# Kernel optimization log

Measured on AMD Instinct MI355X. Metric: run time of the kernel, lower is better.

The kernel has to match this reference:

```python
import jax, jax.numpy as jnp
import numpy as np

N_NODES = 100000


def setup_inputs() -> dict:
    key = jax.random.key(0)
    k1, k2, k3 = jax.random.split(key, 3)
    Cin, Cout, E = 128, 128, 1600000
    x = jax.random.normal(k1, (N_NODES, Cin), dtype=jnp.float32)
    edge_index = jax.random.randint(k2, (2, E), 0, N_NODES, dtype=jnp.int64)
    W = jax.random.normal(k3, (Cin, Cout), dtype=jnp.float32) * 0.05
    b = jnp.zeros((Cout,), dtype=jnp.float32)
    return {"x": x, "edge_index": edge_index, "W": W, "b": b}


def reference(x, edge_index, W, b):
    # GCNConv with self-loops + symmetric normalization, then SiLU.
    N = x.shape[0]
    loops = jnp.arange(N, dtype=edge_index.dtype)
    src = jnp.concatenate([edge_index[0], loops])  # [E+N]
    dst = jnp.concatenate([edge_index[1], loops])  # [E+N]

    h = x @ W  # [N, Cout]

    # degree on dst column (includes self-loops)
    deg = jax.ops.segment_sum(jnp.ones_like(dst, dtype=h.dtype), dst, num_segments=N)
    dis = jnp.where(deg > 0, jax.lax.rsqrt(jnp.maximum(deg, 1.0)), 0.0)  # deg^-1/2, inf->0
    norm = dis[src] * dis[dst]  # [E+N]

    msgs = h[src] * norm[:, None]  # gather + scale
    out = jax.ops.segment_sum(msgs, dst, num_segments=N) + b  # scatter-add
    return jax.nn.silu(out)
```

## Files before the change

### kernel.cpp

```cpp
#include <hip/hip_runtime.h>
#include <math.h>

#define C      128
#define C2U    64
#define BSH    7
#define BNODES 128
#define CHUNKE 6144
#define PADMAX (BNODES * 3)

typedef __attribute__((ext_vector_type(8))) short bf16x8;
typedef __attribute__((ext_vector_type(4))) float f32x4;

union UV { uint4 u; bf16x8 h; };

__device__ __forceinline__ unsigned int f2bf(float f) {
    unsigned int u = __float_as_uint(f);
    return (u + 0x7fffu + ((u >> 16) & 1u)) >> 16;
}
__device__ __forceinline__ float bflo(unsigned int v) { return __uint_as_float(v << 16); }
__device__ __forceinline__ float bfhi(unsigned int v) { return __uint_as_float(v & 0xffff0000u); }

__global__ __launch_bounds__(256) void ngl_chist_kernel(
        const int* __restrict__ dst, int E, int NBUCK, int NBLK, int* __restrict__ cnt) {
    extern __shared__ int h[];
    for (int i = threadIdx.x; i < NBUCK; i += 256) h[i] = 0;
    __syncthreads();
    int base = blockIdx.x * CHUNKE;
    int end = base + CHUNKE; if (end > E) end = E;
    for (int i = base + threadIdx.x; i < end; i += 256)
        atomicAdd(&h[dst[i] >> BSH], 1);
    __syncthreads();
    for (int i = threadIdx.x; i < NBUCK; i += 256)
        cnt[i * NBLK + blockIdx.x] = h[i];
}

__global__ __launch_bounds__(256) void ngl_s1_kernel(const int* __restrict__ in,
                                                     int* __restrict__ bsum, int M,
                                                     const float* __restrict__ W,
                                                     unsigned int* __restrict__ Wt) {
    int g = blockIdx.x * 256 + threadIdx.x;
    if (g < C * C2U) {
        int col = g >> 6, k2 = g & 63;
        float w0 = W[(2 * k2) * C + col];
        float w1 = W[(2 * k2 + 1) * C + col];
        Wt[col * C2U + k2] = f2bf(w0) | (f2bf(w1) << 16);
    }

    __shared__ int red[256];
    int t = threadIdx.x;
    int base = blockIdx.x * 1024 + t * 4;
    int s = 0;
    #pragma unroll
    for (int j = 0; j < 4; ++j) {
        int i = base + j;
        if (i < M) s += in[i];
    }
    red[t] = s;
    __syncthreads();
    for (int o = 128; o > 0; o >>= 1) {
        if (t < o) red[t] += red[t + o];
        __syncthreads();
    }
    if (t == 0) bsum[blockIdx.x] = red[0];
}

__global__ __launch_bounds__(256) void ngl_s2_kernel(
        const int* __restrict__ in, const int* __restrict__ bsum,
        int* __restrict__ out, int M, int NB) {
    __shared__ int pre[256];
    __shared__ int red[256];
    int t = threadIdx.x;
    pre[t] = (t < NB) ? bsum[t] : 0;
    __syncthreads();
    for (int o = 1; o < 256; o <<= 1) {
        int v = 0;
        if (t >= o) v = pre[t - o];
        __syncthreads();
        if (t >= o) pre[t] += v;
        __syncthreads();
    }
    int boff = (blockIdx.x == 0) ? 0 : pre[blockIdx.x - 1];

    int base = blockIdx.x * 1024 + t * 4;
    int v[4];
    int s = 0;
    #pragma unroll
    for (int j = 0; j < 4; ++j) {
        int i = base + j;
        v[j] = (i < M) ? in[i] : 0;
        s += v[j];
    }
    red[t] = s;
    __syncthreads();
    for (int o = 1; o < 256; o <<= 1) {
        int u = 0;
        if (t >= o) u = red[t - o];
        __syncthreads();
        if (t >= o) red[t] += u;
        __syncthreads();
    }
    int run = boff + ((t == 0) ? 0 : red[t - 1]);
    #pragma unroll
    for (int j = 0; j < 4; ++j) {
        int i = base + j;
        if (i < M) {
            out[i] = run;
            run += v[j];
        }
    }
}

__global__ __launch_bounds__(256) void ngl_cscat_kernel(
        const int* __restrict__ src, const int* __restrict__ dst, int E,
        int NBUCK, int NBLK, const int* __restrict__ cntoff,
        unsigned int* __restrict__ pk) {
    extern __shared__ int cur[];
    int blk = blockIdx.x;
    for (int i = threadIdx.x; i < NBUCK; i += 256) cur[i] = cntoff[i * NBLK + blk];
    __syncthreads();
    int base = blk * CHUNKE;
    int end = base + CHUNKE; if (end > E) end = E;
    for (int i = base + threadIdx.x; i < end; i += 256) {
        int d = dst[i];
        int b = d >> BSH;
        int pos = atomicAdd(&cur[b], 1);
        pk[pos] = (unsigned int)src[i] | ((unsigned int)(d & (BNODES - 1)) << 17);
    }
}

__global__ __launch_bounds__(256) void ngl_fcomb_kernel(
        const unsigned int* __restrict__ pk, const int* __restrict__ cntoff,
        int NBLK, int E, int N,
        int* __restrict__ deg, float* __restrict__ dis,
        int* __restrict__ offset, int* __restrict__ payload) {
    __shared__ int h[BNODES];
    __shared__ int sc[BNODES];
    __shared__ int cur[BNODES];
    int b = blockIdx.x, nb = gridDim.x;
    int s = cntoff[b * NBLK];
    int e = (b + 1 < nb) ? cntoff[(b + 1) * NBLK] : E;
    int pbase = s + b * PADMAX;
    int t = threadIdx.x;
    if (t < BNODES) h[t] = 0;
    __syncthreads();
    for (int i = s + t; i < e; i += 256)
        atomicAdd(&h[pk[i] >> 17], 1);
    __syncthreads();
    if (t < BNODES) sc[t] = (h[t] + 3) & ~3;
    __syncthreads();
    for (int o = 1; o < BNODES; o <<= 1) {
        int v = 0;
        if (t < BNODES && t >= o) v = sc[t - o];
        __syncthreads();
        if (t < BNODES && t >= o) sc[t] += v;
        __syncthreads();
    }
    if (t < BNODES) {
        int pc = (h[t] + 3) & ~3;
        int ex = sc[t] - pc;
        cur[t] = ex;
        int n = b * BNODES + t;
        if (n < N) {
            int dv = h[t];
            deg[n] = dv;
            dis[n] = rsqrtf((float)(dv + 1));
            offset[n] = pbase + ex;
        }
    }
    __syncthreads();
    for (int i = s + t; i < e; i += 256) {
        unsigned int p = pk[i];
        int loc = (int)(p >> 17);
        int pos = pbase + atomicAdd(&cur[loc], 1);
        payload[pos] = (int)(p & 0x1FFFFu);
    }
    __syncthreads();
    if (t < BNODES) {
        for (int j = cur[t]; j < sc[t]; ++j)
            payload[pbase + j] = N;
    }
}

__global__ __launch_bounds__(256) void ngl_cvtx_kernel(
        const float4* __restrict__ x4, const float* __restrict__ dis,
        uint4* __restrict__ xh4, int N, int nt) {
    int t = blockIdx.x * blockDim.x + threadIdx.x;
    if (t >= nt) return;
    int node = t >> 4;
    int q = t & 15;
    if (node >= N) {
        xh4[node * 16 + q] = make_uint4(0, 0, 0, 0);
        return;
    }
    float d = dis[node];
    float4 a = x4[node * 32 + q * 2], b = x4[node * 32 + q * 2 + 1];
    uint4 o;
    o.x = f2bf(a.x * d) | (f2bf(a.y * d) << 16);
    o.y = f2bf(a.z * d) | (f2bf(a.w * d) << 16);
    o.z = f2bf(b.x * d) | (f2bf(b.y * d) << 16);
    o.w = f2bf(b.z * d) | (f2bf(b.w * d) << 16);
    xh4[node * 16 + q] = o;
}

__global__ __launch_bounds__(256) void ngl_gather_kernel(
        const unsigned int* __restrict__ xh, const float* __restrict__ dis,
        const int* __restrict__ offset, const int* __restrict__ deg,
        const int* __restrict__ payload, unsigned int* __restrict__ agg, int N) {
    int node = blockIdx.x * 4 + (threadIdx.x >> 6);
    int lane = threadIdx.x & 63;
    if (node >= N) return;

    unsigned int sv = xh[(unsigned int)(node * C2U + lane)];
    float accx = bflo(sv);
    float accy = bfhi(sv);

    int beg = offset[node];
    int cntp = (deg[node] + 3) & ~3;

    if (cntp > 0) {
        int e0 = payload[beg + 0], e1 = payload[beg + 1];
        int e2 = payload[beg + 2], e3 = payload[beg + 3];
        int i = 0;
        while (true) {
            int c0 = e0, c1 = e1, c2 = e2, c3 = e3;
            int nb = beg + i + 4;
            if (i + 8 <= cntp) {
                e0 = payload[nb + 0]; e1 = payload[nb + 1];
                e2 = payload[nb + 2]; e3 = payload[nb + 3];
            }
            unsigned int v0 = xh[(unsigned int)(c0 * C2U + lane)];
            unsigned int v1 = xh[(unsigned int)(c1 * C2U + lane)];
            unsigned int v2 = xh[(unsigned int)(c2 * C2U + lane)];
            unsigned int v3 = xh[(unsigned int)(c3 * C2U + lane)];
            accx += bflo(v0); accy += bfhi(v0);
            accx += bflo(v1); accy += bfhi(v1);
            accx += bflo(v2); accy += bfhi(v2);
            accx += bflo(v3); accy += bfhi(v3);
            i += 4;
            if (i >= cntp) break;
        }
    }
    float dn = dis[node];
    agg[(unsigned int)(node * C2U + lane)] = f2bf(accx * dn) | (f2bf(accy * dn) << 16);
}

__device__ __forceinline__ float silu1(float v) {
    return v / (1.0f + __expf(-v));
}

__global__ __launch_bounds__(256, 2) void ngl_mfma_gemm_kernel(
        const uint4* __restrict__ agg4, const uint4* __restrict__ wt4,
        const float* __restrict__ bias, float* __restrict__ out,
        int N, int tiles_total) {
    int wid  = threadIdx.x >> 6;
    int lane = threadIdx.x & 63;
    int r  = lane & 15;
    int kg = lane >> 4;

    bf16x8 bfr[8][4];
    #pragma unroll
    for (int nt = 0; nt < 8; ++nt) {
        #pragma unroll
        for (int kk = 0; kk < 4; ++kk) {
            UV u; u.u = wt4[(nt * 16 + r) * 16 + kk * 4 + kg];
            bfr[nt][kk] = u.h;
        }
    }
    float bv[8];
    #pragma unroll
    for (int nt = 0; nt < 8; ++nt) bv[nt] = bias[nt * 16 + r];

    for (int tile = blockIdx.x * 4 + wid; tile < tiles_total; tile += gridDim.x * 4) {
        int row0 = tile * 16;
        int arow = row0 + r;

        bf16x8 afr[4];
        #pragma unroll
        for (int kk = 0; kk < 4; ++kk) {
            UV u;
            u.u = (arow < N) ? agg4[(long long)arow * 16 + kk * 4 + kg]
                             : make_uint4(0, 0, 0, 0);
            afr[kk] = u.h;
        }

        f32x4 acc[8];
        #pragma unroll
        for (int nt = 0; nt < 8; ++nt) acc[nt] = (f32x4){0.f, 0.f, 0.f, 0.f};

        #pragma unroll
        for (int kk = 0; kk < 4; ++kk) {
            #pragma unroll
            for (int nt = 0; nt < 8; ++nt) {
                acc[nt] = __builtin_amdgcn_mfma_f32_16x16x32_bf16(
                    afr[kk], bfr[nt][kk], acc[nt], 0, 0, 0);
            }
        }

        #pragma unroll
        for (int nt = 0; nt < 8; ++nt) {
            #pragma unroll
            for (int j = 0; j < 4; ++j) {
                int rr = row0 + kg * 4 + j;
                if (rr < N)
                    __builtin_nontemporal_store(
                        silu1(acc[nt][j] + bv[nt]),
                        &out[(long long)rr * C + nt * 16 + r]);
            }
        }
    }
}

extern "C" void kernel_launch(void* const* d_in, const int* in_sizes, int n_in,
                              void* d_out, int out_size, void* d_ws, size_t ws_size,
                              hipStream_t stream) {
    const float* x = (const float*)d_in[0];
    const int*   ei = (const int*)d_in[1];
    const float* W = (const float*)d_in[2];
    const float* b = (const float*)d_in[3];

    int N = in_sizes[0] / C;
    int E = in_sizes[1] / 2;
    const int* src = ei;
    const int* dst = ei + E;

    int NBUCK = (N + BNODES - 1) / BNODES;
    int NBLK  = (E + CHUNKE - 1) / CHUNKE;
    int M     = NBUCK * NBLK;
    int NB2   = (M + 1023) / 1024;

    char* ws = (char*)d_ws;
    size_t off = 0;
    unsigned int* xh = (unsigned int*)(ws + off);  off += (size_t)(N + 1) * C * 2;
    unsigned int* agg = (unsigned int*)(ws + off); off += (size_t)N * C * 2;
    unsigned int* pk = (unsigned int*)(ws + off);  off += (size_t)E * 4;
    int* payload = (int*)(ws + off);               off += ((size_t)E + (size_t)NBUCK * PADMAX + 1024) * 4;
    int* cnt = (int*)(ws + off);                   off += (size_t)M * 4;
    int* cntoff = (int*)(ws + off);                off += (size_t)M * 4;
    int* s1sum = (int*)(ws + off);                 off += 1024 * 4;
    int* deg = (int*)(ws + off);                   off += (size_t)N * 4;
    int* offset = (int*)(ws + off);                off += (size_t)N * 4;
    float* dis = (float*)(ws + off);               off += (size_t)N * 4;
    unsigned int* Wt = (unsigned int*)(ws + off);  off += (size_t)C * C2U * 4;

    ngl_chist_kernel<<<NBLK, 256, NBUCK * 4, stream>>>(dst, E, NBUCK, NBLK, cnt);
    ngl_s1_kernel<<<NB2, 256, 0, stream>>>(cnt, s1sum, M, W, Wt);
    ngl_s2_kernel<<<NB2, 256, 0, stream>>>(cnt, s1sum, cntoff, M, NB2);
    ngl_cscat_kernel<<<NBLK, 256, NBUCK * 4, stream>>>(src, dst, E, NBUCK, NBLK, cntoff, pk);
    ngl_fcomb_kernel<<<NBUCK, 256, 0, stream>>>(pk, cntoff, NBLK, E, N,
                                                deg, dis, offset, payload);

    int ntx = (N + 1) * 16;
    ngl_cvtx_kernel<<<(ntx + 255) / 256, 256, 0, stream>>>(
        (const float4*)x, dis, (uint4*)xh, N, ntx);

    ngl_gather_kernel<<<(N + 3) / 4, 256, 0, stream>>>(
        xh, dis, offset, deg, payload, agg, N);

    int tiles = (N + 15) / 16;
    ngl_mfma_gemm_kernel<<<512, 256, 0, stream>>>(
        (const uint4*)agg, (const uint4*)Wt, b, (float*)d_out, N, tiles);
}
```

Baseline: 155.0 us.

## Fuse x conversion into CSR build and fuse gather with MFMA GEMM

Folds the x-to-bf16 scaling pass into the per-bucket CSR combine kernel, using degree scales held in shared memory. It also merges the neighbor gather with the MFMA projection: each block aggregates 16 rows into a swizzled LDS tile, then four waves each compute two output column tiles. This removes two launches and the bf16 agg round trip through global memory. The cost is that every block reloads its W fragments, and the GEMM can no longer run as a persistent grid that keeps weights in registers.

```diff
diff --git a/kernel.cpp b/kernel.cpp
--- a/kernel.cpp
+++ b/kernel.cpp
@@ -37,7 +37,8 @@
 __global__ __launch_bounds__(256) void ngl_s1_kernel(const int* __restrict__ in,
                                                      int* __restrict__ bsum, int M,
                                                      const float* __restrict__ W,
-                                                     unsigned int* __restrict__ Wt) {
+                                                     unsigned int* __restrict__ Wt,
+                                                     uint4* __restrict__ xh4, int N) {
     int g = blockIdx.x * 256 + threadIdx.x;
     if (g < C * C2U) {
         int col = g >> 6, k2 = g & 63;
@@ -45,6 +46,8 @@
         float w1 = W[(2 * k2 + 1) * C + col];
         Wt[col * C2U + k2] = f2bf(w0) | (f2bf(w1) << 16);
     }
+    if (blockIdx.x == 0 && threadIdx.x < 16)
+        xh4[(long long)N * 16 + threadIdx.x] = make_uint4(0, 0, 0, 0);
 
     __shared__ int red[256];
     int t = threadIdx.x;
@@ -132,10 +135,12 @@
         const unsigned int* __restrict__ pk, const int* __restrict__ cntoff,
         int NBLK, int E, int N,
         int* __restrict__ deg, float* __restrict__ dis,
-        int* __restrict__ offset, int* __restrict__ payload) {
+        int* __restrict__ offset, int* __restrict__ payload,
+        const float4* __restrict__ x4, uint4* __restrict__ xh4) {
     __shared__ int h[BNODES];
     __shared__ int sc[BNODES];
     __shared__ int cur[BNODES];
+    __shared__ float dl[BNODES];
     int b = blockIdx.x, nb = gridDim.x;
     int s = cntoff[b * NBLK];
     int e = (b + 1 < nb) ? cntoff[(b + 1) * NBLK] : E;
@@ -160,10 +165,12 @@
         int ex = sc[t] - pc;
         cur[t] = ex;
         int n = b * BNODES + t;
+        int dv = h[t];
+        float d = rsqrtf((float)(dv + 1));
+        dl[t] = d;
         if (n < N) {
-            int dv = h[t];
             deg[n] = dv;
-            dis[n] = rsqrtf((float)(dv + 1));
+            dis[n] = d;
             offset[n] = pbase + ex;
         }
     }
@@ -179,133 +186,122 @@
         for (int j = cur[t]; j < sc[t]; ++j)
             payload[pbase + j] = N;
     }
-}
-
-__global__ __launch_bounds__(256) void ngl_cvtx_kernel(
-        const float4* __restrict__ x4, const float* __restrict__ dis,
-        uint4* __restrict__ xh4, int N, int nt) {
-    int t = blockIdx.x * blockDim.x + threadIdx.x;
-    if (t >= nt) return;
-    int node = t >> 4;
     int q = t & 15;
-    if (node >= N) {
-        xh4[node * 16 + q] = make_uint4(0, 0, 0, 0);
-        return;
-    }
-    float d = dis[node];
-    float4 a = x4[node * 32 + q * 2], b = x4[node * 32 + q * 2 + 1];
-    uint4 o;
-    o.x = f2bf(a.x * d) | (f2bf(a.y * d) << 16);
-    o.y = f2bf(a.z * d) | (f2bf(a.w * d) << 16);
-    o.z = f2bf(b.x * d) | (f2bf(b.y * d) << 16);
-    o.w = f2bf(b.z * d) | (f2bf(b.w * d) << 16);
-    xh4[node * 16 + q] = o;
-}
-
-__global__ __launch_bounds__(256) void ngl_gather_kernel(
+    #pragma unroll
+    for (int it = 0; it < 8; ++it) {
+        int rloc = it * 16 + (t >> 4);
+        int n = b * BNODES + rloc;
+        if (n < N) {
+            float d = dl[rloc];
+            float4 a = x4[(long long)n * 32 + q * 2];
+            float4 bb = x4[(long long)n * 32 + q * 2 + 1];
+            uint4 o;
+            o.x = f2bf(a.x * d) | (f2bf(a.y * d) << 16);
+            o.y = f2bf(a.z * d) | (f2bf(a.w * d) << 16);
+            o.z = f2bf(bb.x * d) | (f2bf(bb.y * d) << 16);
+            o.w = f2bf(bb.z * d) | (f2bf(bb.w * d) << 16);
+            xh4[(long long)n * 16 + q] = o;
+        }
+    }
+}
+
+__device__ __forceinline__ float silu1(float v) {
+    return v / (1.0f + __expf(-v));
+}
+
+__global__ __launch_bounds__(256) void ngl_gg_kernel(
         const unsigned int* __restrict__ xh, const float* __restrict__ dis,
         const int* __restrict__ offset, const int* __restrict__ deg,
-        const int* __restrict__ payload, unsigned int* __restrict__ agg, int N) {
-    int node = blockIdx.x * 4 + (threadIdx.x >> 6);
-    int lane = threadIdx.x & 63;
-    if (node >= N) return;
-
-    unsigned int sv = xh[(unsigned int)(node * C2U + lane)];
-    float accx = bflo(sv);
-    float accy = bfhi(sv);
-
-    int beg = offset[node];
-    int cntp = (deg[node] + 3) & ~3;
-
-    if (cntp > 0) {
-        int e0 = payload[beg + 0], e1 = payload[beg + 1];
-        int e2 = payload[beg + 2], e3 = payload[beg + 3];
-        int i = 0;
-        while (true) {
-            int c0 = e0, c1 = e1, c2 = e2, c3 = e3;
-            int nb = beg + i + 4;
-            if (i + 8 <= cntp) {
-                e0 = payload[nb + 0]; e1 = payload[nb + 1];
-                e2 = payload[nb + 2]; e3 = payload[nb + 3];
-            }
-            unsigned int v0 = xh[(unsigned int)(c0 * C2U + lane)];
-            unsigned int v1 = xh[(unsigned int)(c1 * C2U + lane)];
-            unsigned int v2 = xh[(unsigned int)(c2 * C2U + lane)];
-            unsigned int v3 = xh[(unsigned int)(c3 * C2U + lane)];
-            accx += bflo(v0); accy += bfhi(v0);
-            accx += bflo(v1); accy += bfhi(v1);
-            accx += bflo(v2); accy += bfhi(v2);
-            accx += bflo(v3); accy += bfhi(v3);
-            i += 4;
-            if (i >= cntp) break;
-        }
-    }
-    float dn = dis[node];
-    agg[(unsigned int)(node * C2U + lane)] = f2bf(accx * dn) | (f2bf(accy * dn) << 16);
-}
-
-__device__ __forceinline__ float silu1(float v) {
-    return v / (1.0f + __expf(-v));
-}
-
-__global__ __launch_bounds__(256, 2) void ngl_mfma_gemm_kernel(
-        const uint4* __restrict__ agg4, const uint4* __restrict__ wt4,
-        const float* __restrict__ bias, float* __restrict__ out,
-        int N, int tiles_total) {
+        const int* __restrict__ payload,
+        const uint4* __restrict__ wt4, const float* __restrict__ bias,
+        float* __restrict__ out, int N) {
+    __shared__ unsigned int xs[16 * 64];
     int wid  = threadIdx.x >> 6;
     int lane = threadIdx.x & 63;
     int r  = lane & 15;
     int kg = lane >> 4;
 
-    bf16x8 bfr[8][4];
-    #pragma unroll
-    for (int nt = 0; nt < 8; ++nt) {
+    bf16x8 bfr[2][4];
+    float bv[2];
+    #pragma unroll
+    for (int n2 = 0; n2 < 2; ++n2) {
+        int nt = wid * 2 + n2;
         #pragma unroll
         for (int kk = 0; kk < 4; ++kk) {
             UV u; u.u = wt4[(nt * 16 + r) * 16 + kk * 4 + kg];
-            bfr[nt][kk] = u.h;
-        }
-    }
-    float bv[8];
-    #pragma unroll
-    for (int nt = 0; nt < 8; ++nt) bv[nt] = bias[nt * 16 + r];
-
-    for (int tile = blockIdx.x * 4 + wid; tile < tiles_total; tile += gridDim.x * 4) {
-        int row0 = tile * 16;
-        int arow = row0 + r;
-
-        bf16x8 afr[4];
+            bfr[n2][kk] = u.h;
+        }
+        bv[n2] = bias[nt * 16 + r];
+    }
+
+    int row0 = blockIdx.x * 16;
+
+    #pragma unroll
+    for (int j = 0; j < 4; ++j) {
+        int row = wid * 4 + j;
+        int node = row0 + row;
+        float accx = 0.f, accy = 0.f;
+        if (node < N) {
+            unsigned int sv = xh[(unsigned int)(node * C2U + lane)];
+            accx = bflo(sv);
+            accy = bfhi(sv);
+            int beg = offset[node];
+            int cntp = (deg[node] + 3) & ~3;
+            if (cntp > 0) {
+                int e0 = payload[beg + 0], e1 = payload[beg + 1];
+                int e2 = payload[beg + 2], e3 = payload[beg + 3];
+                int i = 0;
+                while (true) {
+                    int c0 = e0, c1 = e1, c2 = e2, c3 = e3;
+                    int nb = beg + i + 4;
+                    if (i + 8 <= cntp) {
+                        e0 = payload[nb + 0]; e1 = payload[nb + 1];
+                        e2 = payload[nb + 2]; e3 = payload[nb + 3];
+                    }
+                    unsigned int v0 = xh[(unsigned int)(c0 * C2U + lane)];
+                    unsigned int v1 = xh[(unsigned int)(c1 * C2U + lane)];
+                    unsigned int v2 = xh[(unsigned int)(c2 * C2U + lane)];
+                    unsigned int v3 = xh[(unsigned int)(c3 * C2U + lane)];
+                    accx += bflo(v0); accy += bfhi(v0);
+                    accx += bflo(v1); accy += bfhi(v1);
+                    accx += bflo(v2); accy += bfhi(v2);
+                    accx += bflo(v3); accy += bfhi(v3);
+                    i += 4;
+                    if (i >= cntp) break;
+                }
+            }
+            float dn = dis[node];
+            accx *= dn; accy *= dn;
+        }
+        xs[row * 64 + ((lane + row * 4) & 63)] = f2bf(accx) | (f2bf(accy) << 16);
+    }
+    __syncthreads();
+
+    bf16x8 afr[4];
+    #pragma unroll
+    for (int kk = 0; kk < 4; ++kk) {
+        UV u;
+        u.u = *(const uint4*)&xs[r * 64 + ((kk * 16 + kg * 4 + r * 4) & 63)];
+        afr[kk] = u.h;
+    }
+    f32x4 acc[2];
+    acc[0] = (f32x4){0.f, 0.f, 0.f, 0.f};
+    acc[1] = (f32x4){0.f, 0.f, 0.f, 0.f};
+    #pragma unroll
+    for (int kk = 0; kk < 4; ++kk) {
+        acc[0] = __builtin_amdgcn_mfma_f32_16x16x32_bf16(afr[kk], bfr[0][kk], acc[0], 0, 0, 0);
+        acc[1] = __builtin_amdgcn_mfma_f32_16x16x32_bf16(afr[kk], bfr[1][kk], acc[1], 0, 0, 0);
+    }
+    #pragma unroll
+    for (int n2 = 0; n2 < 2; ++n2) {
+        int colbase = (wid * 2 + n2) * 16 + r;
         #pragma unroll
-        for (int kk = 0; kk < 4; ++kk) {
-            UV u;
-            u.u = (arow < N) ? agg4[(long long)arow * 16 + kk * 4 + kg]
-                             : make_uint4(0, 0, 0, 0);
-            afr[kk] = u.h;
-        }
-
-        f32x4 acc[8];
-        #pragma unroll
-        for (int nt = 0; nt < 8; ++nt) acc[nt] = (f32x4){0.f, 0.f, 0.f, 0.f};
-
-        #pragma unroll
-        for (int kk = 0; kk < 4; ++kk) {
-            #pragma unroll
-            for (int nt = 0; nt < 8; ++nt) {
-                acc[nt] = __builtin_amdgcn_mfma_f32_16x16x32_bf16(
-                    afr[kk], bfr[nt][kk], acc[nt], 0, 0, 0);
-            }
-        }
-
-        #pragma unroll
-        for (int nt = 0; nt < 8; ++nt) {
-            #pragma unroll
-            for (int j = 0; j < 4; ++j) {
-                int rr = row0 + kg * 4 + j;
-                if (rr < N)
-                    __builtin_nontemporal_store(
-                        silu1(acc[nt][j] + bv[nt]),
-                        &out[(long long)rr * C + nt * 16 + r]);
-            }
+        for (int j = 0; j < 4; ++j) {
+            int rr = row0 + kg * 4 + j;
+            if (rr < N)
+                __builtin_nontemporal_store(
+                    silu1(acc[n2][j] + bv[n2]),
+                    &out[(unsigned int)(rr * C + colbase)]);
         }
     }
 }
@@ -331,7 +327,6 @@
     char* ws = (char*)d_ws;
     size_t off = 0;
     unsigned int* xh = (unsigned int*)(ws + off);  off += (size_t)(N + 1) * C * 2;
-    unsigned int* agg = (unsigned int*)(ws + off); off += (size_t)N * C * 2;
     unsigned int* pk = (unsigned int*)(ws + off);  off += (size_t)E * 4;
     int* payload = (int*)(ws + off);               off += ((size_t)E + (size_t)NBUCK * PADMAX + 1024) * 4;
     int* cnt = (int*)(ws + off);                   off += (size_t)M * 4;
@@ -343,20 +338,14 @@
     unsigned int* Wt = (unsigned int*)(ws + off);  off += (size_t)C * C2U * 4;
 
     ngl_chist_kernel<<<NBLK, 256, NBUCK * 4, stream>>>(dst, E, NBUCK, NBLK, cnt);
-    ngl_s1_kernel<<<NB2, 256, 0, stream>>>(cnt, s1sum, M, W, Wt);
+    ngl_s1_kernel<<<NB2, 256, 0, stream>>>(cnt, s1sum, M, W, Wt, (uint4*)xh, N);
     ngl_s2_kernel<<<NB2, 256, 0, stream>>>(cnt, s1sum, cntoff, M, NB2);
     ngl_cscat_kernel<<<NBLK, 256, NBUCK * 4, stream>>>(src, dst, E, NBUCK, NBLK, cntoff, pk);
     ngl_fcomb_kernel<<<NBUCK, 256, 0, stream>>>(pk, cntoff, NBLK, E, N,
-                                                deg, dis, offset, payload);
-
-    int ntx = (N + 1) * 16;
-    ngl_cvtx_kernel<<<(ntx + 255) / 256, 256, 0, stream>>>(
-        (const float4*)x, dis, (uint4*)xh, N, ntx);
-
-    ngl_gather_kernel<<<(N + 3) / 4, 256, 0, stream>>>(
-        xh, dis, offset, deg, payload, agg, N);
+                                                deg, dis, offset, payload,
+                                                (const float4*)x, (uint4*)xh);
 
     int tiles = (N + 15) / 16;
-    ngl_mfma_gemm_kernel<<<512, 256, 0, stream>>>(
-        (const uint4*)agg, (const uint4*)Wt, b, (float*)d_out, N, tiles);
-}
+    ngl_gg_kernel<<<tiles, 256, 0, stream>>>(
+        xh, dis, offset, deg, payload, (const uint4*)Wt, b, (float*)d_out, N);
+}
```

After: 155.7 us. No clear change (+0.5%).

## Reorder GEMM before aggregation, fusing x conversion into GEMM and SiLU into gather

Applied to the files above, without the earlier changes.

Switches from aggregate-then-transform to transform-then-aggregate. The bf16 conversion of x (scaled by deg^-1/2) now happens inside the MFMA GEMM, which writes h in bf16. The gather kernel then aggregates h rows and applies the destination norm, bias and SiLU, writing the final output directly. This drops the separate cvtx kernel and the agg intermediate round-trip, one launch overall. In exchange, h is rounded to bf16 after the matmul instead of before it, which changes numerics slightly; the 2-byte scattered stores in the GEMM epilogue may be inefficient.

```diff
diff --git a/kernel.cpp b/kernel.cpp
--- a/kernel.cpp
+++ b/kernel.cpp
@@ -37,7 +37,8 @@
 __global__ __launch_bounds__(256) void ngl_s1_kernel(const int* __restrict__ in,
                                                      int* __restrict__ bsum, int M,
                                                      const float* __restrict__ W,
-                                                     unsigned int* __restrict__ Wt) {
+                                                     unsigned int* __restrict__ Wt,
+                                                     uint4* __restrict__ hh4, int N) {
     int g = blockIdx.x * 256 + threadIdx.x;
     if (g < C * C2U) {
         int col = g >> 6, k2 = g & 63;
@@ -45,6 +46,8 @@
         float w1 = W[(2 * k2 + 1) * C + col];
         Wt[col * C2U + k2] = f2bf(w0) | (f2bf(w1) << 16);
     }
+    if (blockIdx.x == 0 && threadIdx.x < 16)
+        hh4[(long long)N * 16 + threadIdx.x] = make_uint4(0, 0, 0, 0);
 
     __shared__ int red[256];
     int t = threadIdx.x;
@@ -181,36 +184,86 @@
     }
 }
 
-__global__ __launch_bounds__(256) void ngl_cvtx_kernel(
+__global__ __launch_bounds__(256, 2) void ngl_gemmcvt_kernel(
         const float4* __restrict__ x4, const float* __restrict__ dis,
-        uint4* __restrict__ xh4, int N, int nt) {
-    int t = blockIdx.x * blockDim.x + threadIdx.x;
-    if (t >= nt) return;
-    int node = t >> 4;
-    int q = t & 15;
-    if (node >= N) {
-        xh4[node * 16 + q] = make_uint4(0, 0, 0, 0);
-        return;
-    }
-    float d = dis[node];
-    float4 a = x4[node * 32 + q * 2], b = x4[node * 32 + q * 2 + 1];
-    uint4 o;
-    o.x = f2bf(a.x * d) | (f2bf(a.y * d) << 16);
-    o.y = f2bf(a.z * d) | (f2bf(a.w * d) << 16);
-    o.z = f2bf(b.x * d) | (f2bf(b.y * d) << 16);
-    o.w = f2bf(b.z * d) | (f2bf(b.w * d) << 16);
-    xh4[node * 16 + q] = o;
+        const uint4* __restrict__ wt4,
+        unsigned short* __restrict__ hh, int N, int tiles_total) {
+    int wid  = threadIdx.x >> 6;
+    int lane = threadIdx.x & 63;
+    int r  = lane & 15;
+    int kg = lane >> 4;
+
+    bf16x8 bfr[8][4];
+    #pragma unroll
+    for (int nt = 0; nt < 8; ++nt) {
+        #pragma unroll
+        for (int kk = 0; kk < 4; ++kk) {
+            UV u; u.u = wt4[(nt * 16 + r) * 16 + kk * 4 + kg];
+            bfr[nt][kk] = u.h;
+        }
+    }
+
+    for (int tile = blockIdx.x * 4 + wid; tile < tiles_total; tile += gridDim.x * 4) {
+        int row0 = tile * 16;
+        int arow = row0 + r;
+        float d = (arow < N) ? dis[arow] : 0.f;
+
+        bf16x8 afr[4];
+        #pragma unroll
+        for (int kk = 0; kk < 4; ++kk) {
+            float4 a = make_float4(0, 0, 0, 0), bb = make_float4(0, 0, 0, 0);
+            if (arow < N) {
+                a  = x4[(long long)arow * 32 + kk * 8 + kg * 2];
+                bb = x4[(long long)arow * 32 + kk * 8 + kg * 2 + 1];
+            }
+            UV u;
+            u.u.x = f2bf(a.x * d) | (f2bf(a.y * d) << 16);
+            u.u.y = f2bf(a.z * d) | (f2bf(a.w * d) << 16);
+            u.u.z = f2bf(bb.x * d) | (f2bf(bb.y * d) << 16);
+            u.u.w = f2bf(bb.z * d) | (f2bf(bb.w * d) << 16);
+            afr[kk] = u.h;
+        }
+
+        f32x4 acc[8];
+        #pragma unroll
+        for (int nt = 0; nt < 8; ++nt) acc[nt] = (f32x4){0.f, 0.f, 0.f, 0.f};
+
+        #pragma unroll
+        for (int kk = 0; kk < 4; ++kk) {
+            #pragma unroll
+            for (int nt = 0; nt < 8; ++nt) {
+                acc[nt] = __builtin_amdgcn_mfma_f32_16x16x32_bf16(
+                    afr[kk], bfr[nt][kk], acc[nt], 0, 0, 0);
+            }
+        }
+
+        #pragma unroll
+        for (int nt = 0; nt < 8; ++nt) {
+            #pragma unroll
+            for (int j = 0; j < 4; ++j) {
+                int rr = row0 + kg * 4 + j;
+                if (rr < N)
+                    hh[(long long)rr * C + nt * 16 + r] =
+                        (unsigned short)f2bf(acc[nt][j]);
+            }
+        }
+    }
+}
+
+__device__ __forceinline__ float silu1(float v) {
+    return v / (1.0f + __expf(-v));
 }
 
 __global__ __launch_bounds__(256) void ngl_gather_kernel(
-        const unsigned int* __restrict__ xh, const float* __restrict__ dis,
+        const unsigned int* __restrict__ hh, const float* __restrict__ dis,
         const int* __restrict__ offset, const int* __restrict__ deg,
-        const int* __restrict__ payload, unsigned int* __restrict__ agg, int N) {
+        const int* __restrict__ payload, const float* __restrict__ bias,
+        float* __restrict__ out, int N) {
     int node = blockIdx.x * 4 + (threadIdx.x >> 6);
     int lane = threadIdx.x & 63;
     if (node >= N) return;
 
-    unsigned int sv = xh[(unsigned int)(node * C2U + lane)];
+    unsigned int sv = hh[(unsigned int)(node * C2U + lane)];
     float accx = bflo(sv);
     float accy = bfhi(sv);
 
@@ -228,10 +281,10 @@
                 e0 = payload[nb + 0]; e1 = payload[nb + 1];
                 e2 = payload[nb + 2]; e3 = payload[nb + 3];
             }
-            unsigned int v0 = xh[(unsigned int)(c0 * C2U + lane)];
-            unsigned int v1 = xh[(unsigned int)(c1 * C2U + lane)];
-            unsigned int v2 = xh[(unsigned int)(c2 * C2U + lane)];
-            unsigned int v3 = xh[(unsigned int)(c3 * C2U + lane)];
+            unsigned int v0 = hh[(unsigned int)(c0 * C2U + lane)];
+            unsigned int v1 = hh[(unsigned int)(c1 * C2U + lane)];
+            unsigned int v2 = hh[(unsigned int)(c2 * C2U + lane)];
+            unsigned int v3 = hh[(unsigned int)(c3 * C2U + lane)];
             accx += bflo(v0); accy += bfhi(v0);
             accx += bflo(v1); accy += bfhi(v1);
             accx += bflo(v2); accy += bfhi(v2);
@@ -241,73 +294,11 @@
         }
     }
     float dn = dis[node];
-    agg[(unsigned int)(node * C2U + lane)] = f2bf(accx * dn) | (f2bf(accy * dn) << 16);
-}
-
-__device__ __forceinline__ float silu1(float v) {
-    return v / (1.0f + __expf(-v));
-}
-
-__global__ __launch_bounds__(256, 2) void ngl_mfma_gemm_kernel(
-        const uint4* __restrict__ agg4, const uint4* __restrict__ wt4,
-        const float* __restrict__ bias, float* __restrict__ out,
-        int N, int tiles_total) {
-    int wid  = threadIdx.x >> 6;
-    int lane = threadIdx.x & 63;
-    int r  = lane & 15;
-    int kg = lane >> 4;
-
-    bf16x8 bfr[8][4];
-    #pragma unroll
-    for (int nt = 0; nt < 8; ++nt) {
-        #pragma unroll
-        for (int kk = 0; kk < 4; ++kk) {
-            UV u; u.u = wt4[(nt * 16 + r) * 16 + kk * 4 + kg];
-            bfr[nt][kk] = u.h;
-        }
-    }
-    float bv[8];
-    #pragma unroll
-    for (int nt = 0; nt < 8; ++nt) bv[nt] = bias[nt * 16 + r];
-
-    for (int tile = blockIdx.x * 4 + wid; tile < tiles_total; tile += gridDim.x * 4) {
-        int row0 = tile * 16;
-        int arow = row0 + r;
-
-        bf16x8 afr[4];
-        #pragma unroll
-        for (int kk = 0; kk < 4; ++kk) {
-            UV u;
-            u.u = (arow < N) ? agg4[(long long)arow * 16 + kk * 4 + kg]
-                             : make_uint4(0, 0, 0, 0);
-            afr[kk] = u.h;
-        }
-
-        f32x4 acc[8];
-        #pragma unroll
-        for (int nt = 0; nt < 8; ++nt) acc[nt] = (f32x4){0.f, 0.f, 0.f, 0.f};
-
-        #pragma unroll
-        for (int kk = 0; kk < 4; ++kk) {
-            #pragma unroll
-            for (int nt = 0; nt < 8; ++nt) {
-                acc[nt] = __builtin_amdgcn_mfma_f32_16x16x32_bf16(
-                    afr[kk], bfr[nt][kk], acc[nt], 0, 0, 0);
-            }
-        }
-
-        #pragma unroll
-        for (int nt = 0; nt < 8; ++nt) {
-            #pragma unroll
-            for (int j = 0; j < 4; ++j) {
-                int rr = row0 + kg * 4 + j;
-                if (rr < N)
-                    __builtin_nontemporal_store(
-                        silu1(acc[nt][j] + bv[nt]),
-                        &out[(long long)rr * C + nt * 16 + r]);
-            }
-        }
-    }
+    float2 bb = ((const float2*)bias)[lane];
+    float ox = silu1(accx * dn + bb.x);
+    float oy = silu1(accy * dn + bb.y);
+    __builtin_nontemporal_store(ox, &out[(unsigned int)(node * C + 2 * lane)]);
+    __builtin_nontemporal_store(oy, &out[(unsigned int)(node * C + 2 * lane + 1)]);
 }
 
 extern "C" void kernel_launch(void* const* d_in, const int* in_sizes, int n_in,
@@ -330,8 +321,7 @@
 
     char* ws = (char*)d_ws;
     size_t off = 0;
-    unsigned int* xh = (unsigned int*)(ws + off);  off += (size_t)(N + 1) * C * 2;
-    unsigned int* agg = (unsigned int*)(ws + off); off += (size_t)N * C * 2;
+    unsigned short* hh = (unsigned short*)(ws + off); off += (size_t)(N + 1) * C * 2;
     unsigned int* pk = (unsigned int*)(ws + off);  off += (size_t)E * 4;
     int* payload = (int*)(ws + off);               off += ((size_t)E + (size_t)NBUCK * PADMAX + 1024) * 4;
     int* cnt = (int*)(ws + off);                   off += (size_t)M * 4;
@@ -343,20 +333,16 @@
     unsigned int* Wt = (unsigned int*)(ws + off);  off += (size_t)C * C2U * 4;
 
     ngl_chist_kernel<<<NBLK, 256, NBUCK * 4, stream>>>(dst, E, NBUCK, NBLK, cnt);
-    ngl_s1_kernel<<<NB2, 256, 0, stream>>>(cnt, s1sum, M, W, Wt);
+    ngl_s1_kernel<<<NB2, 256, 0, stream>>>(cnt, s1sum, M, W, Wt, (uint4*)hh, N);
     ngl_s2_kernel<<<NB2, 256, 0, stream>>>(cnt, s1sum, cntoff, M, NB2);
     ngl_cscat_kernel<<<NBLK, 256, NBUCK * 4, stream>>>(src, dst, E, NBUCK, NBLK, cntoff, pk);
     ngl_fcomb_kernel<<<NBUCK, 256, 0, stream>>>(pk, cntoff, NBLK, E, N,
                                                 deg, dis, offset, payload);
 
-    int ntx = (N + 1) * 16;
-    ngl_cvtx_kernel<<<(ntx + 255) / 256, 256, 0, stream>>>(
-        (const float4*)x, dis, (uint4*)xh, N, ntx);
+    int tiles = (N + 15) / 16;
+    ngl_gemmcvt_kernel<<<512, 256, 0, stream>>>(
+        (const float4*)x, dis, (const uint4*)Wt, hh, N, tiles);
 
     ngl_gather_kernel<<<(N + 3) / 4, 256, 0, stream>>>(
-        xh, dis, offset, deg, payload, agg, N);
-
-    int tiles = (N + 15) / 16;
-    ngl_mfma_gemm_kernel<<<512, 256, 0, stream>>>(
-        (const uint4*)agg, (const uint4*)Wt, b, (float*)d_out, N, tiles);
-}
+        (const unsigned int*)hh, dis, offset, deg, payload, b, (float*)d_out, N);
+}
```

New measurement: 144.1 us, median of 2. 1.08x faster.
